# Kernel tuning notes

Measured on AMD Instinct MI355X. Metric: run time of the kernel, lower is better.

Reference implementation:

```python
import jax, jax.numpy as jnp
import numpy as np

ALPHA = 0.1        # dt / tau = 1 / 10
SIGMA_REC = 0.03
SIGMA_INP = 0.03


def setup_inputs() -> dict:
    key = jax.random.key(0)
    ks = jax.random.split(key, 7)
    n, N, num_inputs, num_outputs, T, B = 128, 1024, 6, 2, 512, 256
    u = jax.random.normal(ks[0], (num_inputs, T, B), dtype=jnp.float32)
    rec_noise = jax.random.normal(ks[1], (B, T, n), dtype=jnp.float32)
    inp_noise = jax.random.normal(ks[2], (B, T, num_inputs), dtype=jnp.float32)
    W_inp = jax.random.normal(ks[3], (n, num_inputs), dtype=jnp.float32) / np.float32(np.sqrt(num_inputs))
    # spectral-ish scaling keeps the leaky RNN stable over 512 steps
    W_rec = jax.random.normal(ks[4], (n, n), dtype=jnp.float32) * np.float32(0.9 / np.sqrt(n))
    W_out = jax.random.normal(ks[5], (num_outputs, n), dtype=jnp.float32) / np.float32(np.sqrt(n))
    # q is orthonormalized via SVD in the torch module (make_orthonormal)
    q0 = np.asarray(jax.random.uniform(ks[6], (n, N)), dtype=np.float32)
    U, _, Vh = np.linalg.svd(q0, full_matrices=False)
    q = jnp.asarray((U @ Vh).astype(np.float32))
    return dict(u=u, rec_noise=rec_noise, inp_noise=inp_noise,
                W_inp=W_inp, W_rec=W_rec, W_out=W_out, q=q)


def reference(u, rec_noise, inp_noise, W_inp, W_rec, W_out, q):
    # u: (num_inputs, T, B); noise tensors already batch-major (B, T, .)
    B = u.shape[-1]
    n = W_rec.shape[0]
    rn = jnp.sqrt(2.0 / ALPHA * SIGMA_REC ** 2) * rec_noise      # (B, T, n)
    inoise = jnp.sqrt(2.0 / ALPHA * SIGMA_INP ** 2) * inp_noise  # (B, T, num_inputs)
    ub = jnp.swapaxes(u, 0, -1)                                  # (B, T, num_inputs)
    x0 = jnp.zeros((B, n), dtype=u.dtype)                        # initial state self.x = 0

    def step(x, ins):
        u_t, in_t, rn_t = ins
        x_new = (1.0 - ALPHA) * x + ALPHA * (
            jax.nn.relu(x @ W_rec.T + (u_t + in_t) @ W_inp.T) + rn_t)
        return x_new, x_new

    # T-1 update steps using inputs at t = 0 .. T-2 (matches the torch loop)
    xs_in = (jnp.swapaxes(ub, 0, 1)[:-1],
             jnp.swapaxes(inoise, 0, 1)[:-1],
             jnp.swapaxes(rn, 0, 1)[:-1])
    _, xs = jax.lax.scan(step, x0, xs_in)                        # (T-1, B, n)
    states = jnp.concatenate([x0[:, None, :], jnp.swapaxes(xs, 0, 1)], axis=1)  # (B, T, n)

    outputs = jnp.swapaxes(states @ W_out.T, 0, -1)              # (num_outputs, T, B)
    states_embedded = jnp.swapaxes(states @ q, 0, -1)            # (N, T, B)
    return states_embedded, outputs
```

## Files before the change

### kernel.cpp

```cpp
#include <hip/hip_runtime.h>
#include <hip/hip_bf16.h>

#define T_STEPS 512
#define BATCH   256
#define NN      128
#define NEMB    1024
#define M_ROWS  (T_STEPS * BATCH)
#define NOISE_K 0.13416407864998738f
#define CH      8
#define NCHUNK  (T_STEPS / CH)

typedef short s16x8 __attribute__((ext_vector_type(8)));
typedef float f32x4 __attribute__((ext_vector_type(4)));

__device__ __forceinline__ unsigned short f2bf(float f) {
  union { float f; unsigned u; } v; v.f = f;
  unsigned r = v.u + 0x7fffu + ((v.u >> 16) & 1u);
  return (unsigned short)(r >> 16);
}
__device__ __forceinline__ float bf2f(unsigned short s) {
  union { unsigned u; float f; } v; v.u = ((unsigned)s) << 16;
  return v.f;
}

__global__ __launch_bounds__(256, 1) void rnn_step_kernel(
    const float* __restrict__ u,
    const float* __restrict__ rec_noise,
    const float* __restrict__ inp_noise,
    const float* __restrict__ W_inp,
    const float* __restrict__ W_rec,
    unsigned short* __restrict__ states)
{
  const int b   = blockIdx.x;
  const int tid = threadIdx.x;
  const int i   = tid >> 1;
  const int h   = tid & 1;

  __shared__ float xbuf[2][136];
  __shared__ float rns[2][CH * NN];
  __shared__ float us[2][CH][8];

  const float4* wr = (const float4*)(W_rec + i * NN + h * 64);
  const float4 w0 = wr[0],  w1 = wr[1],  w2 = wr[2],  w3 = wr[3];
  const float4 w4 = wr[4],  w5 = wr[5],  w6 = wr[6],  w7 = wr[7];
  const float4 w8 = wr[8],  w9 = wr[9],  wA = wr[10], wB = wr[11];
  const float4 wC = wr[12], wD = wr[13], wE = wr[14], wF = wr[15];

  float winp[6];
  #pragma unroll
  for (int j = 0; j < 6; ++j) winp[j] = W_inp[i * 6 + j];

  const int ts6 = tid / 6, j6 = tid - ts6 * 6;

  if (tid < 136) xbuf[0][tid] = 0.f;
  if (h == 0) states[b * NN + i] = 0;

  {
    const f32x4* src = (const f32x4*)(rec_noise + (size_t)b * T_STEPS * NN);
    *(f32x4*)&rns[0][tid * 4] = src[tid];
    if (tid < 48) {
      float uu = u[j6 * (T_STEPS * BATCH) + ts6 * BATCH + b];
      float in = inp_noise[((size_t)b * T_STEPS + ts6) * 6 + j6];
      us[0][ts6][j6] = uu + NOISE_K * in;
    }
  }
  __syncthreads();

  float xr = 0.f;
  for (int c = 0; c < NCHUNK; ++c) {
    const int cb = c & 1;

    f32x4 rn_pf = {0.f, 0.f, 0.f, 0.f};
    float u_pf = 0.f, in_pf = 0.f;
    if (c < NCHUNK - 1) {
      const f32x4* src =
          (const f32x4*)(rec_noise + ((size_t)b * T_STEPS + (c + 1) * CH) * NN);
      rn_pf = src[tid];
      if (tid < 48) {
        const int tt = (c + 1) * CH + ts6;
        u_pf  = u[j6 * (T_STEPS * BATCH) + tt * BATCH + b];
        in_pf = inp_noise[((size_t)b * T_STEPS + tt) * 6 + j6];
      }
    }

    #pragma unroll
    for (int ts = 0; ts < CH; ++ts) {
      const int t = c * CH + ts;
      if (t > T_STEPS - 2) break;
      const int cur = ts & 1, nxt = cur ^ 1;

      const float* xb = &xbuf[cur][h * 68];
      float a0 = 0.f, a1 = 0.f, a2 = 0.f, a3 = 0.f;
      #define STEP4(W, IDX, ACC)                                  \
        { float4 xv = *(const float4*)&xb[(IDX) * 4];             \
          ACC = fmaf(W.x, xv.x, ACC); ACC = fmaf(W.y, xv.y, ACC); \
          ACC = fmaf(W.z, xv.z, ACC); ACC = fmaf(W.w, xv.w, ACC); }
      STEP4(w0, 0, a0) STEP4(w1, 1, a1) STEP4(w2, 2, a2) STEP4(w3, 3, a3)
      STEP4(w4, 4, a0) STEP4(w5, 5, a1) STEP4(w6, 6, a2) STEP4(w7, 7, a3)
      STEP4(w8, 8, a0) STEP4(w9, 9, a1) STEP4(wA, 10, a2) STEP4(wB, 11, a3)
      STEP4(wC, 12, a0) STEP4(wD, 13, a1) STEP4(wE, 14, a2) STEP4(wF, 15, a3)
      #undef STEP4
      float acc = (a0 + a1) + (a2 + a3);
      acc += __shfl_xor(acc, 1);

      float inp = 0.f;
      #pragma unroll
      for (int j = 0; j < 6; ++j) inp = fmaf(winp[j], us[cb][ts][j], inp);

      const float pre = acc + inp;
      const float r   = pre > 0.f ? pre : 0.f;
      const float xn  = 0.9f * xr + 0.1f * (r + NOISE_K * rns[cb][ts * NN + i]);
      xr = xn;

      if (h == 0) {
        xbuf[nxt][i + ((i >> 6) << 2)] = xn;
        states[((t + 1) * BATCH + b) * NN + i] = f2bf(xn);
      }
      __syncthreads();
    }

    if (c < NCHUNK - 1) {
      *(f32x4*)&rns[cb ^ 1][tid * 4] = rn_pf;
      if (tid < 48) us[cb ^ 1][ts6][j6] = u_pf + NOISE_K * in_pf;
      __syncthreads();
    }
  }
}

__global__ __launch_bounds__(256) void emb_kernel(
    const unsigned short* __restrict__ states,
    const float* __restrict__ q,
    const float* __restrict__ W_out,
    float* __restrict__ out)
{
  const int jt  = blockIdx.x;
  const int mt  = blockIdx.y;
  const int tid = threadIdx.x;
  const int w   = tid >> 6;
  const int l   = tid & 63;
  const int lg  = l >> 4;
  const int lr  = l & 15;

  __shared__ unsigned short qt[64 * 128];
  __shared__ float tr[64 * 132];
  __shared__ float wos[2 * NN];

  {
    const int j  = tid & 63;
    const int k0 = tid >> 6;
    #pragma unroll
    for (int kk = k0; kk < 128; kk += 4) {
      float v = q[kk * NEMB + jt * 64 + j];
      int k8 = kk >> 3, e = kk & 7;
      qt[j * 128 + ((k8 ^ (j & 7)) << 3) + e] = f2bf(v);
    }
  }
  if (jt == 0) wos[tid] = W_out[tid];

  s16x8 afrag[2][4];
  #pragma unroll
  for (int mf = 0; mf < 2; ++mf) {
    const int m = mt * 128 + w * 32 + mf * 16 + lr;
    const unsigned short* arow = states + m * NN;
    #pragma unroll
    for (int kc = 0; kc < 4; ++kc)
      afrag[mf][kc] = *(const s16x8*)(arow + kc * 32 + lg * 8);
  }
  __syncthreads();

  f32x4 acc[2][4] = {};
  #pragma unroll
  for (int kc = 0; kc < 4; ++kc) {
    s16x8 bfrag[4];
    #pragma unroll
    for (int jf = 0; jf < 4; ++jf) {
      const int jl = jf * 16 + lr;
      bfrag[jf] = *(const s16x8*)(qt + jl * 128 + ((((kc << 2) + lg) ^ (jl & 7)) << 3));
    }
    #pragma unroll
    for (int mf = 0; mf < 2; ++mf)
      #pragma unroll
      for (int jf = 0; jf < 4; ++jf)
        acc[mf][jf] = __builtin_amdgcn_mfma_f32_16x16x32_bf16(
            afrag[mf][kc], bfrag[jf], acc[mf][jf], 0, 0, 0);
  }

  if (jt == 0) {
    #pragma unroll
    for (int mf = 0; mf < 2; ++mf) {
      float s0 = 0.f, s1 = 0.f;
      #pragma unroll
      for (int kc = 0; kc < 4; ++kc) {
        const int kb = kc * 32 + lg * 8;
        const s16x8 af = afrag[mf][kc];
        #pragma unroll
        for (int e = 0; e < 8; ++e) {
          const float x = bf2f((unsigned short)af[e]);
          s0 = fmaf(x, wos[kb + e], s0);
          s1 = fmaf(x, wos[NN + kb + e], s1);
        }
      }
      s0 += __shfl_xor(s0, 16); s0 += __shfl_xor(s0, 32);
      s1 += __shfl_xor(s1, 16); s1 += __shfl_xor(s1, 32);
      if (lg == 0) {
        const long m = (long)mt * 128 + w * 32 + mf * 16 + lr;
        out[(long)1024 * M_ROWS + m] = s0;
        out[(long)1025 * M_ROWS + m] = s1;
      }
    }
  }

  #pragma unroll
  for (int mf = 0; mf < 2; ++mf) {
    const int m0 = w * 32 + mf * 16 + lg * 4;
    #pragma unroll
    for (int jf = 0; jf < 4; ++jf)
      *(f32x4*)&tr[(jf * 16 + lr) * 132 + m0] = acc[mf][jf];
  }
  __syncthreads();

  const int mo = (tid & 31) * 4;
  #pragma unroll
  for (int p = 0; p < 8; ++p) {
    const int jr = p * 8 + (tid >> 5);
    f32x4 v = *(const f32x4*)&tr[jr * 132 + mo];
    *(f32x4*)&out[(long)(jt * 64 + jr) * M_ROWS + mt * 128 + mo] = v;
  }
}

extern "C" void kernel_launch(void* const* d_in, const int* in_sizes, int n_in,
                              void* d_out, int out_size, void* d_ws, size_t ws_size,
                              hipStream_t stream) {
  const float* u         = (const float*)d_in[0];
  const float* rec_noise = (const float*)d_in[1];
  const float* inp_noise = (const float*)d_in[2];
  const float* W_inp     = (const float*)d_in[3];
  const float* W_rec     = (const float*)d_in[4];
  const float* W_out     = (const float*)d_in[5];
  const float* q         = (const float*)d_in[6];
  float* out = (float*)d_out;
  unsigned short* states = (unsigned short*)d_ws;

  rnn_step_kernel<<<dim3(BATCH), dim3(256), 0, stream>>>(
      u, rec_noise, inp_noise, W_inp, W_rec, states);

  dim3 g2(NEMB / 64, M_ROWS / 128);
  emb_kernel<<<g2, dim3(256), 0, stream>>>(states, q, W_out, out);
}
```

Before: 457.5 us.

## Use one thread per state row with readlane broadcast and lighter barriers

The recurrent kernel now runs 128 threads per batch element, one per hidden unit, each holding its full W_rec row in registers. The state vector is broadcast with readlane instead of LDS float4 reads, the pair shuffle is gone, and __syncthreads is replaced by a raw s_barrier that only waits on LDS counters. The embedding kernel also drops its LDS transpose and writes MFMA accumulators straight to global memory. Costs: 128 weight registers per thread, serial readlane latency, and less coalesced output stores in the GEMM.

```diff
diff --git a/kernel.cpp b/kernel.cpp
--- a/kernel.cpp
+++ b/kernel.cpp
@@ -22,8 +22,17 @@
   union { unsigned u; float f; } v; v.u = ((unsigned)s) << 16;
   return v.f;
 }
-
-__global__ __launch_bounds__(256, 1) void rnn_step_kernel(
+__device__ __forceinline__ float rdlane(float v, int l) {
+  return __uint_as_float(__builtin_amdgcn_readlane(__float_as_uint(v), l));
+}
+
+__device__ __forceinline__ void light_barrier() {
+  asm volatile("s_waitcnt lgkmcnt(0)" ::: "memory");
+  __builtin_amdgcn_s_barrier();
+  asm volatile("" ::: "memory");
+}
+
+__global__ __launch_bounds__(128, 1) void rnn_step_kernel(
     const float* __restrict__ u,
     const float* __restrict__ rec_noise,
     const float* __restrict__ inp_noise,
@@ -31,33 +40,32 @@
     const float* __restrict__ W_rec,
     unsigned short* __restrict__ states)
 {
-  const int b   = blockIdx.x;
-  const int tid = threadIdx.x;
-  const int i   = tid >> 1;
-  const int h   = tid & 1;
-
-  __shared__ float xbuf[2][136];
+  const int b    = blockIdx.x;
+  const int tid  = threadIdx.x;
+  const int lane = tid & 63;
+
+  __shared__ float xbuf[2][NN];
   __shared__ float rns[2][CH * NN];
   __shared__ float us[2][CH][8];
 
-  const float4* wr = (const float4*)(W_rec + i * NN + h * 64);
-  const float4 w0 = wr[0],  w1 = wr[1],  w2 = wr[2],  w3 = wr[3];
-  const float4 w4 = wr[4],  w5 = wr[5],  w6 = wr[6],  w7 = wr[7];
-  const float4 w8 = wr[8],  w9 = wr[9],  wA = wr[10], wB = wr[11];
-  const float4 wC = wr[12], wD = wr[13], wE = wr[14], wF = wr[15];
+  const f32x4* wr = (const f32x4*)(W_rec + tid * NN);
+  f32x4 w4[32];
+  #pragma unroll
+  for (int c = 0; c < 32; ++c) w4[c] = wr[c];
 
   float winp[6];
   #pragma unroll
-  for (int j = 0; j < 6; ++j) winp[j] = W_inp[i * 6 + j];
+  for (int j = 0; j < 6; ++j) winp[j] = W_inp[tid * 6 + j];
 
   const int ts6 = tid / 6, j6 = tid - ts6 * 6;
 
-  if (tid < 136) xbuf[0][tid] = 0.f;
-  if (h == 0) states[b * NN + i] = 0;
+  xbuf[0][tid] = 0.f;
+  states[b * NN + tid] = 0;
 
   {
     const f32x4* src = (const f32x4*)(rec_noise + (size_t)b * T_STEPS * NN);
-    *(f32x4*)&rns[0][tid * 4] = src[tid];
+    *(f32x4*)&rns[0][tid * 8]     = src[tid * 2];
+    *(f32x4*)&rns[0][tid * 8 + 4] = src[tid * 2 + 1];
     if (tid < 48) {
       float uu = u[j6 * (T_STEPS * BATCH) + ts6 * BATCH + b];
       float in = inp_noise[((size_t)b * T_STEPS + ts6) * 6 + j6];
@@ -70,12 +78,13 @@
   for (int c = 0; c < NCHUNK; ++c) {
     const int cb = c & 1;
 
-    f32x4 rn_pf = {0.f, 0.f, 0.f, 0.f};
+    f32x4 pf0 = {0.f, 0.f, 0.f, 0.f}, pf1 = {0.f, 0.f, 0.f, 0.f};
     float u_pf = 0.f, in_pf = 0.f;
     if (c < NCHUNK - 1) {
       const f32x4* src =
           (const f32x4*)(rec_noise + ((size_t)b * T_STEPS + (c + 1) * CH) * NN);
-      rn_pf = src[tid];
+      pf0 = src[tid * 2];
+      pf1 = src[tid * 2 + 1];
       if (tid < 48) {
         const int tt = (c + 1) * CH + ts6;
         u_pf  = u[j6 * (T_STEPS * BATCH) + tt * BATCH + b];
@@ -89,19 +98,19 @@
       if (t > T_STEPS - 2) break;
       const int cur = ts & 1, nxt = cur ^ 1;
 
-      const float* xb = &xbuf[cur][h * 68];
+      float2 vx = *(const float2*)&xbuf[cur][lane * 2];
+
       float a0 = 0.f, a1 = 0.f, a2 = 0.f, a3 = 0.f;
-      #define STEP4(W, IDX, ACC)                                  \
-        { float4 xv = *(const float4*)&xb[(IDX) * 4];             \
-          ACC = fmaf(W.x, xv.x, ACC); ACC = fmaf(W.y, xv.y, ACC); \
-          ACC = fmaf(W.z, xv.z, ACC); ACC = fmaf(W.w, xv.w, ACC); }
-      STEP4(w0, 0, a0) STEP4(w1, 1, a1) STEP4(w2, 2, a2) STEP4(w3, 3, a3)
-      STEP4(w4, 4, a0) STEP4(w5, 5, a1) STEP4(w6, 6, a2) STEP4(w7, 7, a3)
-      STEP4(w8, 8, a0) STEP4(w9, 9, a1) STEP4(wA, 10, a2) STEP4(wB, 11, a3)
-      STEP4(wC, 12, a0) STEP4(wD, 13, a1) STEP4(wE, 14, a2) STEP4(wF, 15, a3)
-      #undef STEP4
+      #pragma unroll
+      for (int kp = 0; kp < 64; ++kp) {
+        const float x0 = rdlane(vx.x, kp);
+        const float x1 = rdlane(vx.y, kp);
+        const float we0 = w4[kp >> 1][(kp & 1) * 2];
+        const float we1 = w4[kp >> 1][(kp & 1) * 2 + 1];
+        if (kp & 1) { a2 = fmaf(we0, x0, a2); a3 = fmaf(we1, x1, a3); }
+        else        { a0 = fmaf(we0, x0, a0); a1 = fmaf(we1, x1, a1); }
+      }
       float acc = (a0 + a1) + (a2 + a3);
-      acc += __shfl_xor(acc, 1);
 
       float inp = 0.f;
       #pragma unroll
@@ -109,20 +118,20 @@
 
       const float pre = acc + inp;
       const float r   = pre > 0.f ? pre : 0.f;
-      const float xn  = 0.9f * xr + 0.1f * (r + NOISE_K * rns[cb][ts * NN + i]);
+      const float xn  = 0.9f * xr + 0.1f * (r + NOISE_K * rns[cb][ts * NN + tid]);
       xr = xn;
 
-      if (h == 0) {
-        xbuf[nxt][i + ((i >> 6) << 2)] = xn;
-        states[((t + 1) * BATCH + b) * NN + i] = f2bf(xn);
-      }
-      __syncthreads();
+      xbuf[nxt][tid] = xn;
+      states[((t + 1) * BATCH + b) * NN + tid] = f2bf(xn);
+
+      light_barrier();
     }
 
     if (c < NCHUNK - 1) {
-      *(f32x4*)&rns[cb ^ 1][tid * 4] = rn_pf;
+      *(f32x4*)&rns[cb ^ 1][tid * 8]     = pf0;
+      *(f32x4*)&rns[cb ^ 1][tid * 8 + 4] = pf1;
       if (tid < 48) us[cb ^ 1][ts6][j6] = u_pf + NOISE_K * in_pf;
-      __syncthreads();
+      light_barrier();
     }
   }
 }
@@ -142,7 +151,6 @@
   const int lr  = l & 15;
 
   __shared__ unsigned short qt[64 * 128];
-  __shared__ float tr[64 * 132];
   __shared__ float wos[2 * NN];
 
   {
@@ -212,19 +220,12 @@
 
   #pragma unroll
   for (int mf = 0; mf < 2; ++mf) {
-    const int m0 = w * 32 + mf * 16 + lg * 4;
-    #pragma unroll
-    for (int jf = 0; jf < 4; ++jf)
-      *(f32x4*)&tr[(jf * 16 + lr) * 132 + m0] = acc[mf][jf];
-  }
-  __syncthreads();
-
-  const int mo = (tid & 31) * 4;
-  #pragma unroll
-  for (int p = 0; p < 8; ++p) {
-    const int jr = p * 8 + (tid >> 5);
-    f32x4 v = *(const f32x4*)&tr[jr * 132 + mo];
-    *(f32x4*)&out[(long)(jt * 64 + jr) * M_ROWS + mt * 128 + mo] = v;
+    const int m = mt * 128 + w * 32 + mf * 16 + lg * 4;
+    #pragma unroll
+    for (int jf = 0; jf < 4; ++jf) {
+      const long j = jt * 64 + jf * 16 + lr;
+      *(f32x4*)&out[j * M_ROWS + m] = acc[mf][jf];
+    }
   }
 }
 
@@ -241,7 +242,7 @@
   float* out = (float*)d_out;
   unsigned short* states = (unsigned short*)d_ws;
 
-  rnn_step_kernel<<<dim3(BATCH), dim3(256), 0, stream>>>(
+  rnn_step_kernel<<<dim3(BATCH), dim3(128), 0, stream>>>(
       u, rec_noise, inp_noise, W_inp, W_rec, states);
 
   dim3 g2(NEMB / 64, M_ROWS / 128);
```

Result: slower. 467.7 us (+2.2%).
